# Kernel optimization log

Hardware: AMD Instinct MI355X
Metric: run time of the kernel (lower is better)

The kernel has to match this reference:

```python
import jax, jax.numpy as jnp
import numpy as np

N = 4_194_304  # total points
C = 2          # classes: 0=ground, 1=plant
B = 8          # number of point clouds in the batch
SIGMA_L = 0.1
SIGMA_R = 0.4
CLAMP_FACTOR = 2.0
MIN_VAL = 0.1
FOCAL_GAMMA = 2.0
FOCAL_ALPHA = 1.0
LOSS_WEIGHT = 1.0


def setup_inputs() -> dict:
    key = jax.random.key(0)
    k1, k2, k3 = jax.random.split(key, 3)
    pred = jax.random.normal(k1, (N, C), dtype=jnp.float32)
    coord = jax.random.normal(k2, (N, 3), dtype=jnp.float32)
    segment = jax.random.randint(k3, (N,), 0, C, dtype=jnp.int32)
    # pointcept-style cumulative offsets: equal-sized clouds, offset[-1] == N
    offset = (jnp.arange(1, B + 1, dtype=jnp.int32) * (N // B))
    return {"pred": pred, "coord": coord, "segment": segment, "offset": offset}


def _gauss_weights(z, segment, batch):
    # per-cloud z_ground_max (fallback: z.min) and z_plant_min (fallback: z.max)
    neg_inf = jnp.array(-jnp.inf, z.dtype)
    pos_inf = jnp.array(jnp.inf, z.dtype)
    gmax = jax.ops.segment_max(jnp.where(segment == 0, z, neg_inf), batch, num_segments=B)
    pmin = jax.ops.segment_min(jnp.where(segment == 1, z, pos_inf), batch, num_segments=B)
    has_g = jax.ops.segment_sum((segment == 0).astype(z.dtype), batch, num_segments=B) > 0
    has_p = jax.ops.segment_sum((segment == 1).astype(z.dtype), batch, num_segments=B) > 0
    zmin = jax.ops.segment_min(z, batch, num_segments=B)
    zmax = jax.ops.segment_max(z, batch, num_segments=B)
    g = jnp.where(has_g, gmax, zmin)
    p = jnp.where(has_p, pmin, zmax)
    mu_b = g + (p - g) * 0.5  # (B,)
    mu = mu_b[batch]          # (N,)
    d = z - mu
    w_left = jnp.exp(-(d * d) / (2.0 * SIGMA_L * SIGMA_L))
    w_right = jnp.exp(-(d * d) / (2.0 * SIGMA_R * SIGMA_R))
    w_right = jnp.where(d > CLAMP_FACTOR * SIGMA_R, jnp.array(MIN_VAL, z.dtype), w_right)
    return jnp.where(z <= mu, w_left, w_right)


def reference(pred, coord, segment, offset):
    n = pred.shape[0]
    # offset2batch: per-point batch id from cumulative offsets
    batch = jnp.searchsorted(offset, jnp.arange(n, dtype=offset.dtype), side='right')
    # cross entropy (reduction='none')
    logp = jax.nn.log_softmax(pred, axis=1)              # (N, C)
    logp_t = jnp.take_along_axis(logp, segment[:, None], axis=1)[:, 0]  # (N,)
    seg_loss = (-logp_t) * LOSS_WEIGHT
    # focal reweighting (computed under no_grad in the original)
    p_t = jax.lax.stop_gradient(jnp.exp(logp_t))
    focal_weight = FOCAL_ALPHA * (1.0 - p_t) ** FOCAL_GAMMA
    seg_loss = seg_loss * focal_weight
    # asymmetric gaussian z-weighting, segment-conditioned per cloud
    weights = _gauss_weights(coord[:, 2], segment, batch)
    return jnp.mean(seg_loss * weights)
```

## Files before the change

### kernel.cpp

```cpp
#include <hip/hip_runtime.h>
#include <math.h>

#define THREADS 256
#define NBLOCKS 256
#define UNROLL  8

__device__ __forceinline__ unsigned enc_f(float f) {
    unsigned b = __float_as_uint(f);
    return (b & 0x80000000u) ? ~b : (b | 0x80000000u);
}
__device__ __forceinline__ float dec_f(unsigned u) {
    unsigned b = (u & 0x80000000u) ? (u ^ 0x80000000u) : ~u;
    return __uint_as_float(b);
}
#define ENC_NEG_INF 0x007FFFFFu
#define ENC_POS_INF 0xFF800000u


__global__ void k_init(unsigned* __restrict__ ws) {
    int t = threadIdx.x;
    if (t < 32) ws[t] = (t < 8 || t >= 24) ? ENC_NEG_INF : ENC_POS_INF;
    else if (t == 32) { *(double*)(ws + 32) = 0.0; ws[34] = 0u; }
}

#define FLUSH_TO(bb, g_, p_, mn_, mx_) do { \
    atomicMax(&s_stats[      (bb)], enc_f(g_));  \
    atomicMin(&s_stats[ 8  + (bb)], enc_f(p_));  \
    atomicMin(&s_stats[16  + (bb)], enc_f(mn_)); \
    atomicMax(&s_stats[24  + (bb)], enc_f(mx_)); } while (0)

__global__ __launch_bounds__(THREADS) void k_stats(
        const float* __restrict__ coord, const int* __restrict__ segment,
        const int* __restrict__ offset, unsigned* __restrict__ ws, int n, int nb) {
    __shared__ unsigned s_stats[32];
    const int tid = threadIdx.x;
    if (tid < 32) s_stats[tid] = (tid < 8 || tid >= 24) ? ENC_NEG_INF : ENC_POS_INF;
    int roff[8];
    #pragma unroll
    for (int j = 0; j < 8; ++j) roff[j] = (j < nb) ? offset[j] : 0x7FFFFFFF;
    __syncthreads();

    const int chunk = (n + (int)gridDim.x - 1) / (int)gridDim.x;
    const int start = blockIdx.x * chunk;
    const int end   = min(n, start + chunk);

    float lg = -INFINITY, lp = INFINITY, lmn = INFINITY, lmx = -INFINITY;

    if (start < end) {
        int ba = 0, bb = 0;
        #pragma unroll
        for (int j = 0; j < 8; ++j) { ba += (start >= roff[j]); bb += ((end - 1) >= roff[j]); }
        if (ba == bb) {
            int i = start + tid;
            for (; i + (UNROLL - 1) * THREADS < end; i += UNROLL * THREADS) {
                float z[UNROLL]; int s[UNROLL];
                #pragma unroll
                for (int k = 0; k < UNROLL; ++k) z[k] = coord[3 * (i + k * THREADS) + 2];
                #pragma unroll
                for (int k = 0; k < UNROLL; ++k) s[k] = segment[i + k * THREADS];
                #pragma unroll
                for (int k = 0; k < UNROLL; ++k) {
                    lmn = fminf(lmn, z[k]);
                    lmx = fmaxf(lmx, z[k]);
                    lg  = fmaxf(lg, (s[k] == 0) ? z[k] : -INFINITY);
                    lp  = fminf(lp, (s[k] != 0) ? z[k] : INFINITY);
                }
            }
            for (; i < end; i += THREADS) {
                float z = coord[3 * i + 2]; int s = segment[i];
                lmn = fminf(lmn, z); lmx = fmaxf(lmx, z);
                lg  = fmaxf(lg, (s == 0) ? z : -INFINITY);
                lp  = fminf(lp, (s != 0) ? z : INFINITY);
            }
            #pragma unroll
            for (int m = 32; m; m >>= 1) {
                lg  = fmaxf(lg,  __shfl_xor(lg,  m, 64));
                lp  = fminf(lp,  __shfl_xor(lp,  m, 64));
                lmn = fminf(lmn, __shfl_xor(lmn, m, 64));
                lmx = fmaxf(lmx, __shfl_xor(lmx, m, 64));
            }
            if ((tid & 63) == 0) FLUSH_TO(ba, lg, lp, lmn, lmx);
        } else {
            int curb = -1;
            for (int i = start + tid; i < end; i += THREADS) {
                float z = coord[3 * i + 2]; int s = segment[i], b = 0;
                #pragma unroll
                for (int j = 0; j < 8; ++j) b += (i >= roff[j]);
                if (b != curb) {
                    if (curb >= 0) FLUSH_TO(curb, lg, lp, lmn, lmx);
                    lg = -INFINITY; lp = INFINITY; lmn = INFINITY; lmx = -INFINITY;
                    curb = b;
                }
                lmn = fminf(lmn, z); lmx = fmaxf(lmx, z);
                if (s == 0) lg = fmaxf(lg, z); else lp = fminf(lp, z);
            }
            if (curb >= 0) FLUSH_TO(curb, lg, lp, lmn, lmx);
        }
    }
    __syncthreads();
    if (tid < 32) {
        unsigned v = s_stats[tid];
        unsigned ident = (tid < 8 || tid >= 24) ? ENC_NEG_INF : ENC_POS_INF;
        if (v != ident) {
            if (tid >= 8 && tid < 24) atomicMin(&ws[tid], v);
            else                      atomicMax(&ws[tid], v);
        }
    }
}

__device__ __forceinline__ float point_loss(float p0, float p1, int s, float z, float mu) {
    float m   = fmaxf(p0, p1);
    float lse = m + logf(expf(p0 - m) + expf(p1 - m));
    float lpt = ((s == 0) ? p0 : p1) - lse;
    float pt  = expf(lpt);
    float om  = 1.0f - pt;
    float loss = -lpt * om * om;
    float d  = z - mu;
    float cf = (z <= mu) ? 50.0f : 3.125f;
    float w  = expf(-d * d * cf);
    if (z > mu && d > 0.8f) w = 0.1f;
    return loss * w;
}

__global__ __launch_bounds__(THREADS) void k_loss(
        const float* __restrict__ pred, const float* __restrict__ coord,
        const int* __restrict__ segment, const int* __restrict__ offset,
        unsigned* __restrict__ ws, float* __restrict__ out, int n, int nb) {
    __shared__ float s_mu[8];
    __shared__ float s_part[THREADS / 64];
    const int tid = threadIdx.x;
    int roff[8];
    #pragma unroll
    for (int j = 0; j < 8; ++j) roff[j] = (j < nb) ? offset[j] : 0x7FFFFFFF;
    if (tid < 8) {
        unsigned ug = ws[tid], up = ws[8 + tid];
        float g = dec_f(ug), p = dec_f(up);
        if (ug == ENC_NEG_INF) g = dec_f(ws[16 + tid]);
        if (up == ENC_POS_INF) p = dec_f(ws[24 + tid]);
        s_mu[tid] = g + (p - g) * 0.5f;
    }
    __syncthreads();

    const int chunk = (n + (int)gridDim.x - 1) / (int)gridDim.x;
    const int start = blockIdx.x * chunk;
    const int end   = min(n, start + chunk);
    const float2* pred2 = (const float2*)pred;

    float lsum = 0.0f;
    if (start < end) {
        int ba = 0, bb = 0;
        #pragma unroll
        for (int j = 0; j < 8; ++j) { ba += (start >= roff[j]); bb += ((end - 1) >= roff[j]); }
        if (ba == bb) {
            const float mu = s_mu[ba];
            int i = start + tid;
            for (; i + (UNROLL - 1) * THREADS < end; i += UNROLL * THREADS) {
                float z[UNROLL]; int s[UNROLL]; float2 pp[UNROLL];
                #pragma unroll
                for (int k = 0; k < UNROLL; ++k) pp[k] = pred2[i + k * THREADS];
                #pragma unroll
                for (int k = 0; k < UNROLL; ++k) z[k] = coord[3 * (i + k * THREADS) + 2];
                #pragma unroll
                for (int k = 0; k < UNROLL; ++k) s[k] = segment[i + k * THREADS];
                #pragma unroll
                for (int k = 0; k < UNROLL; ++k)
                    lsum += point_loss(pp[k].x, pp[k].y, s[k], z[k], mu);
            }
            for (; i < end; i += THREADS) {
                float2 pp = pred2[i];
                lsum += point_loss(pp.x, pp.y, segment[i], coord[3 * i + 2], mu);
            }
        } else {
            for (int i = start + tid; i < end; i += THREADS) {
                int b = 0;
                #pragma unroll
                for (int j = 0; j < 8; ++j) b += (i >= roff[j]);
                float2 pp = pred2[i];
                lsum += point_loss(pp.x, pp.y, segment[i], coord[3 * i + 2], s_mu[b]);
            }
        }
    }

    #pragma unroll
    for (int off = 32; off > 0; off >>= 1) lsum += __shfl_down(lsum, off, 64);
    if ((tid & 63) == 0) s_part[tid >> 6] = lsum;
    __syncthreads();
    if (tid == 0) {
        float t = 0.0f;
        #pragma unroll
        for (int wv = 0; wv < THREADS / 64; ++wv) t += s_part[wv];
        double* acc = (double*)(ws + 32);
        atomicAdd(acc, (double)t);
        __threadfence();
        unsigned c = atomicAdd(&ws[34], 1u);
        if (c == (unsigned)gridDim.x - 1u) {
            double v = atomicAdd(acc, 0.0);
            out[0] = (float)(v / (double)n);
        }
    }
}

extern "C" void kernel_launch(void* const* d_in, const int* in_sizes, int n_in,
                              void* d_out, int out_size, void* d_ws, size_t ws_size,
                              hipStream_t stream) {
    const float* pred    = (const float*)d_in[0];
    const float* coord   = (const float*)d_in[1];
    const int*   segment = (const int*)d_in[2];
    const int*   offset  = (const int*)d_in[3];
    const int n  = in_sizes[2];
    const int nb = in_sizes[3];

    unsigned* ws = (unsigned*)d_ws;

    hipLaunchKernelGGL(k_init,  dim3(1), dim3(64), 0, stream, ws);
    hipLaunchKernelGGL(k_stats, dim3(NBLOCKS), dim3(THREADS), 0, stream,
                       coord, segment, offset, ws, n, nb);
    hipLaunchKernelGGL(k_loss,  dim3(NBLOCKS), dim3(THREADS), 0, stream,
                       pred, coord, segment, offset, ws, (float*)d_out, n, nb);
}
```

Measured before the change: 141.6 us.

## Fuse stats and loss kernels with a grid barrier, keeping z and segment in registers

Merges the per-cloud stats kernel and the loss kernel into one persistent kernel. Blocks meet at a global atomic-counter barrier before computing mu. In the fast path each thread keeps its 64 z values in registers and packs its segment labels into a 64-bit mask, so coord and segment are read once instead of twice. This removes one kernel launch and roughly a third of the global traffic. In exchange it relies on all 256 blocks being co-resident for the spin barrier, and the register arrays raise register pressure.

```diff
diff --git a/kernel.cpp b/kernel.cpp
--- a/kernel.cpp
+++ b/kernel.cpp
@@ -3,7 +3,9 @@
 
 #define THREADS 256
 #define NBLOCKS 256
-#define UNROLL  8
+#define ROUNDS  8
+#define U       8
+#define CHUNK   (ROUNDS * U * THREADS)
 
 __device__ __forceinline__ unsigned enc_f(float f) {
     unsigned b = __float_as_uint(f);
@@ -20,93 +22,17 @@
 __global__ void k_init(unsigned* __restrict__ ws) {
     int t = threadIdx.x;
     if (t < 32) ws[t] = (t < 8 || t >= 24) ? ENC_NEG_INF : ENC_POS_INF;
-    else if (t == 32) { *(double*)(ws + 32) = 0.0; ws[34] = 0u; }
+    else if (t == 32) { *(double*)(ws + 32) = 0.0; ws[34] = 0u; ws[35] = 0u; }
 }
 
-#define FLUSH_TO(bb, g_, p_, mn_, mx_) do { \
-    atomicMax(&s_stats[      (bb)], enc_f(g_));  \
-    atomicMin(&s_stats[ 8  + (bb)], enc_f(p_));  \
-    atomicMin(&s_stats[16  + (bb)], enc_f(mn_)); \
-    atomicMax(&s_stats[24  + (bb)], enc_f(mx_)); } while (0)
+#define CNT_B(ii, bdst) do { bdst = 0; \
+    _Pragma("unroll") for (int j_ = 0; j_ < 8; ++j_) bdst += ((ii) >= roff[j_]); } while (0)
 
-__global__ __launch_bounds__(THREADS) void k_stats(
-        const float* __restrict__ coord, const int* __restrict__ segment,
-        const int* __restrict__ offset, unsigned* __restrict__ ws, int n, int nb) {
-    __shared__ unsigned s_stats[32];
-    const int tid = threadIdx.x;
-    if (tid < 32) s_stats[tid] = (tid < 8 || tid >= 24) ? ENC_NEG_INF : ENC_POS_INF;
-    int roff[8];
-    #pragma unroll
-    for (int j = 0; j < 8; ++j) roff[j] = (j < nb) ? offset[j] : 0x7FFFFFFF;
-    __syncthreads();
-
-    const int chunk = (n + (int)gridDim.x - 1) / (int)gridDim.x;
-    const int start = blockIdx.x * chunk;
-    const int end   = min(n, start + chunk);
-
-    float lg = -INFINITY, lp = INFINITY, lmn = INFINITY, lmx = -INFINITY;
-
-    if (start < end) {
-        int ba = 0, bb = 0;
-        #pragma unroll
-        for (int j = 0; j < 8; ++j) { ba += (start >= roff[j]); bb += ((end - 1) >= roff[j]); }
-        if (ba == bb) {
-            int i = start + tid;
-            for (; i + (UNROLL - 1) * THREADS < end; i += UNROLL * THREADS) {
-                float z[UNROLL]; int s[UNROLL];
-                #pragma unroll
-                for (int k = 0; k < UNROLL; ++k) z[k] = coord[3 * (i + k * THREADS) + 2];
-                #pragma unroll
-                for (int k = 0; k < UNROLL; ++k) s[k] = segment[i + k * THREADS];
-                #pragma unroll
-                for (int k = 0; k < UNROLL; ++k) {
-                    lmn = fminf(lmn, z[k]);
-                    lmx = fmaxf(lmx, z[k]);
-                    lg  = fmaxf(lg, (s[k] == 0) ? z[k] : -INFINITY);
-                    lp  = fminf(lp, (s[k] != 0) ? z[k] : INFINITY);
-                }
-            }
-            for (; i < end; i += THREADS) {
-                float z = coord[3 * i + 2]; int s = segment[i];
-                lmn = fminf(lmn, z); lmx = fmaxf(lmx, z);
-                lg  = fmaxf(lg, (s == 0) ? z : -INFINITY);
-                lp  = fminf(lp, (s != 0) ? z : INFINITY);
-            }
-            #pragma unroll
-            for (int m = 32; m; m >>= 1) {
-                lg  = fmaxf(lg,  __shfl_xor(lg,  m, 64));
-                lp  = fminf(lp,  __shfl_xor(lp,  m, 64));
-                lmn = fminf(lmn, __shfl_xor(lmn, m, 64));
-                lmx = fmaxf(lmx, __shfl_xor(lmx, m, 64));
-            }
-            if ((tid & 63) == 0) FLUSH_TO(ba, lg, lp, lmn, lmx);
-        } else {
-            int curb = -1;
-            for (int i = start + tid; i < end; i += THREADS) {
-                float z = coord[3 * i + 2]; int s = segment[i], b = 0;
-                #pragma unroll
-                for (int j = 0; j < 8; ++j) b += (i >= roff[j]);
-                if (b != curb) {
-                    if (curb >= 0) FLUSH_TO(curb, lg, lp, lmn, lmx);
-                    lg = -INFINITY; lp = INFINITY; lmn = INFINITY; lmx = -INFINITY;
-                    curb = b;
-                }
-                lmn = fminf(lmn, z); lmx = fmaxf(lmx, z);
-                if (s == 0) lg = fmaxf(lg, z); else lp = fminf(lp, z);
-            }
-            if (curb >= 0) FLUSH_TO(curb, lg, lp, lmn, lmx);
-        }
-    }
-    __syncthreads();
-    if (tid < 32) {
-        unsigned v = s_stats[tid];
-        unsigned ident = (tid < 8 || tid >= 24) ? ENC_NEG_INF : ENC_POS_INF;
-        if (v != ident) {
-            if (tid >= 8 && tid < 24) atomicMin(&ws[tid], v);
-            else                      atomicMax(&ws[tid], v);
-        }
-    }
-}
+#define FLUSH_G(bb, g_, p_, mn_, mx_) do { \
+    atomicMax(&ws[      (bb)], enc_f(g_));  \
+    atomicMin(&ws[ 8  + (bb)], enc_f(p_));  \
+    atomicMin(&ws[16  + (bb)], enc_f(mn_)); \
+    atomicMax(&ws[24  + (bb)], enc_f(mx_)); } while (0)
 
 __device__ __forceinline__ float point_loss(float p0, float p1, int s, float z, float mu) {
     float m   = fmaxf(p0, p1);
@@ -122,62 +48,116 @@
     return loss * w;
 }
 
-__global__ __launch_bounds__(THREADS) void k_loss(
+__global__ __launch_bounds__(THREADS) void k_fused(
         const float* __restrict__ pred, const float* __restrict__ coord,
         const int* __restrict__ segment, const int* __restrict__ offset,
         unsigned* __restrict__ ws, float* __restrict__ out, int n, int nb) {
-    __shared__ float s_mu[8];
-    __shared__ float s_part[THREADS / 64];
+    __shared__ float    s_mu[8];
+    __shared__ float    s_part[THREADS / 64];
+    __shared__ unsigned s_raw[32];
     const int tid = threadIdx.x;
     int roff[8];
     #pragma unroll
     for (int j = 0; j < 8; ++j) roff[j] = (j < nb) ? offset[j] : 0x7FFFFFFF;
+
+    const int chunk = (n + (int)gridDim.x - 1) / (int)gridDim.x;
+    const int start = blockIdx.x * chunk;
+    const int end   = min(n, start + chunk);
+
+    int ba = 0, bz = 0;
+    if (start < end) {
+        #pragma unroll
+        for (int j = 0; j < 8; ++j) { ba += (start >= roff[j]); bz += ((end - 1) >= roff[j]); }
+    }
+    const bool fast = (start < end) && (ba == bz) && (end - start == CHUNK) && (chunk == CHUNK);
+
+    float zc[ROUNDS][U];
+    unsigned long long segb = 0ull;
+    float lg = -INFINITY, lp = INFINITY, lmn = INFINITY, lmx = -INFINITY;
+
+    if (fast) {
+        #pragma unroll
+        for (int r = 0; r < ROUNDS; ++r) {
+            const int base = start + tid + r * U * THREADS;
+            int sk[U];
+            #pragma unroll
+            for (int k = 0; k < U; ++k) zc[r][k] = coord[3 * (base + k * THREADS) + 2];
+            #pragma unroll
+            for (int k = 0; k < U; ++k) sk[k] = segment[base + k * THREADS];
+            #pragma unroll
+            for (int k = 0; k < U; ++k) {
+                const float z = zc[r][k];
+                lmn = fminf(lmn, z); lmx = fmaxf(lmx, z);
+                lg  = fmaxf(lg, (sk[k] == 0) ? z : -INFINITY);
+                lp  = fminf(lp, (sk[k] != 0) ? z : INFINITY);
+                segb |= ((unsigned long long)(sk[k] & 1)) << (r * U + k);
+            }
+        }
+        #pragma unroll
+        for (int m = 32; m; m >>= 1) {
+            lg  = fmaxf(lg,  __shfl_xor(lg,  m, 64));
+            lp  = fminf(lp,  __shfl_xor(lp,  m, 64));
+            lmn = fminf(lmn, __shfl_xor(lmn, m, 64));
+            lmx = fmaxf(lmx, __shfl_xor(lmx, m, 64));
+        }
+        if ((tid & 63) == 0) FLUSH_G(ba, lg, lp, lmn, lmx);
+    } else if (start < end) {
+        int curb = -1;
+        for (int i = start + tid; i < end; i += THREADS) {
+            float z = coord[3 * i + 2]; int s = segment[i], b;
+            CNT_B(i, b);
+            if (b != curb) {
+                if (curb >= 0) FLUSH_G(curb, lg, lp, lmn, lmx);
+                lg = -INFINITY; lp = INFINITY; lmn = INFINITY; lmx = -INFINITY;
+                curb = b;
+            }
+            lmn = fminf(lmn, z); lmx = fmaxf(lmx, z);
+            if (s == 0) lg = fmaxf(lg, z); else lp = fminf(lp, z);
+        }
+        if (curb >= 0) FLUSH_G(curb, lg, lp, lmn, lmx);
+    }
+
+    __syncthreads();
+    if (tid == 0) {
+        atomicAdd(&ws[35], 1u);
+        int tries = 1 << 22;
+        while (atomicAdd(&ws[35], 0u) < (unsigned)gridDim.x && --tries)
+            __builtin_amdgcn_s_sleep(8);
+        __threadfence();
+    }
+    __syncthreads();
+
+    if (tid < 32) s_raw[tid] = atomicOr(&ws[tid], 0u);
+    __syncthreads();
     if (tid < 8) {
-        unsigned ug = ws[tid], up = ws[8 + tid];
+        unsigned ug = s_raw[tid], up = s_raw[8 + tid];
         float g = dec_f(ug), p = dec_f(up);
-        if (ug == ENC_NEG_INF) g = dec_f(ws[16 + tid]);
-        if (up == ENC_POS_INF) p = dec_f(ws[24 + tid]);
+        if (ug == ENC_NEG_INF) g = dec_f(s_raw[16 + tid]);
+        if (up == ENC_POS_INF) p = dec_f(s_raw[24 + tid]);
         s_mu[tid] = g + (p - g) * 0.5f;
     }
     __syncthreads();
 
-    const int chunk = (n + (int)gridDim.x - 1) / (int)gridDim.x;
-    const int start = blockIdx.x * chunk;
-    const int end   = min(n, start + chunk);
+    float lsum = 0.0f;
     const float2* pred2 = (const float2*)pred;
-
-    float lsum = 0.0f;
-    if (start < end) {
-        int ba = 0, bb = 0;
+    if (fast) {
+        const float mu = s_mu[ba];
         #pragma unroll
-        for (int j = 0; j < 8; ++j) { ba += (start >= roff[j]); bb += ((end - 1) >= roff[j]); }
-        if (ba == bb) {
-            const float mu = s_mu[ba];
-            int i = start + tid;
-            for (; i + (UNROLL - 1) * THREADS < end; i += UNROLL * THREADS) {
-                float z[UNROLL]; int s[UNROLL]; float2 pp[UNROLL];
-                #pragma unroll
-                for (int k = 0; k < UNROLL; ++k) pp[k] = pred2[i + k * THREADS];
-                #pragma unroll
-                for (int k = 0; k < UNROLL; ++k) z[k] = coord[3 * (i + k * THREADS) + 2];
-                #pragma unroll
-                for (int k = 0; k < UNROLL; ++k) s[k] = segment[i + k * THREADS];
-                #pragma unroll
-                for (int k = 0; k < UNROLL; ++k)
-                    lsum += point_loss(pp[k].x, pp[k].y, s[k], z[k], mu);
-            }
-            for (; i < end; i += THREADS) {
-                float2 pp = pred2[i];
-                lsum += point_loss(pp.x, pp.y, segment[i], coord[3 * i + 2], mu);
-            }
-        } else {
-            for (int i = start + tid; i < end; i += THREADS) {
-                int b = 0;
-                #pragma unroll
-                for (int j = 0; j < 8; ++j) b += (i >= roff[j]);
-                float2 pp = pred2[i];
-                lsum += point_loss(pp.x, pp.y, segment[i], coord[3 * i + 2], s_mu[b]);
-            }
+        for (int r = 0; r < ROUNDS; ++r) {
+            const int base = start + tid + r * U * THREADS;
+            float2 pp[U];
+            #pragma unroll
+            for (int k = 0; k < U; ++k) pp[k] = pred2[base + k * THREADS];
+            #pragma unroll
+            for (int k = 0; k < U; ++k)
+                lsum += point_loss(pp[k].x, pp[k].y,
+                                   (int)((segb >> (r * U + k)) & 1ull), zc[r][k], mu);
+        }
+    } else if (start < end) {
+        for (int i = start + tid; i < end; i += THREADS) {
+            int b; CNT_B(i, b);
+            float2 pp = pred2[i];
+            lsum += point_loss(pp.x, pp.y, segment[i], coord[3 * i + 2], s_mu[b]);
         }
     }
 
@@ -213,8 +193,6 @@
     unsigned* ws = (unsigned*)d_ws;
 
     hipLaunchKernelGGL(k_init,  dim3(1), dim3(64), 0, stream, ws);
-    hipLaunchKernelGGL(k_stats, dim3(NBLOCKS), dim3(THREADS), 0, stream,
-                       coord, segment, offset, ws, n, nb);
-    hipLaunchKernelGGL(k_loss,  dim3(NBLOCKS), dim3(THREADS), 0, stream,
+    hipLaunchKernelGGL(k_fused, dim3(NBLOCKS), dim3(THREADS), 0, stream,
                        pred, coord, segment, offset, ws, (float*)d_out, n, nb);
 }
```

New measurement: 161.3 us. 1.14x slower.
